# Kernel tuning notes

Measured on AMD Instinct MI355X. Metric: run time of the kernel, lower is better.

The kernel has to match this reference:

```python
import jax, jax.numpy as jnp
import numpy as np

D = 2048
H = 16
DH = D // H  # 128
B = 512
EPS = 1e-5


def _layernorm(x, g, b):
    m = jnp.mean(x, axis=-1, keepdims=True)
    v = jnp.mean((x - m) ** 2, axis=-1, keepdims=True)
    return (x - m) * jax.lax.rsqrt(v + EPS) * g + b


def setup_inputs() -> dict:
    key = jax.random.key(0)
    ks = jax.random.split(key, 16)
    s_in = 1.0 / np.sqrt(D)
    s_ff = 1.0 / np.sqrt(4 * D)
    return {
        "x": jax.random.normal(ks[0], (B, D), jnp.float32),
        # per-head q/k/v projections, stacked over heads: [H, D, DH]
        "Wq": jax.random.uniform(ks[1], (H, D, DH), jnp.float32, -s_in, s_in),
        "bq": jax.random.uniform(ks[2], (H, DH), jnp.float32, -s_in, s_in),
        "Wk": jax.random.uniform(ks[3], (H, D, DH), jnp.float32, -s_in, s_in),
        "bk": jax.random.uniform(ks[4], (H, DH), jnp.float32, -s_in, s_in),
        "Wv": jax.random.uniform(ks[5], (H, D, DH), jnp.float32, -s_in, s_in),
        "bv": jax.random.uniform(ks[6], (H, DH), jnp.float32, -s_in, s_in),
        "Wo": jax.random.uniform(ks[7], (D, D), jnp.float32, -s_in, s_in),
        "bo": jax.random.uniform(ks[8], (D,), jnp.float32, -s_in, s_in),
        "W1": jax.random.uniform(ks[9], (D, 4 * D), jnp.float32, -s_in, s_in),
        "b1": jax.random.uniform(ks[10], (4 * D,), jnp.float32, -s_in, s_in),
        "W2": jax.random.uniform(ks[11], (4 * D, D), jnp.float32, -s_ff, s_ff),
        "b2": jax.random.uniform(ks[12], (D,), jnp.float32, -s_ff, s_ff),
        "g1": jnp.ones((D,), jnp.float32),
        "be1": jnp.zeros((D,), jnp.float32),
        "g2": jnp.ones((D,), jnp.float32),
        "be2": jnp.zeros((D,), jnp.float32),
    }


def reference(x, Wq, bq, Wk, bk, Wv, bv, Wo, bo, W1, b1, W2, b2, g1, be1, g2, be2):
    # --- pre-norm attention branch ---
    h = _layernorm(x, g1, be1)                       # [B, D]
    q = jnp.einsum('bd,hde->bhe', h, Wq) + bq        # [B, H, DH]
    k = jnp.einsum('bd,hde->bhe', h, Wk) + bk
    v = jnp.einsum('bd,hde->bhe', h, Wv) + bv
    # outer-product 'attention' per sample: [B, H, DH, DH]
    attn = q[..., :, None] * k[..., None, :] / jnp.sqrt(jnp.float32(DH))
    attn = jax.nn.softmax(attn, axis=-1)
    o = jnp.einsum('bhij,bhj->bhi', attn, v)         # [B, H, DH]
    o = o.reshape(x.shape[0], H * DH)                # concat over heads
    x = x + o @ Wo + bo
    # --- pre-norm FFN branch ---
    h2 = _layernorm(x, g2, be2)
    x = x + jax.nn.relu(h2 @ W1 + b1) @ W2 + b2
    return x
```

## Files before the change

kernel.cpp:

```cpp
#include <hip/hip_runtime.h>
#include <hip/hip_bf16.h>
#include <math.h>


#define DDIM 2048
#define HHEADS 16
#define DHEAD 128
#define BROWS 512
#define LN_EPS 1e-5f

typedef __bf16 bf16x8_t __attribute__((ext_vector_type(8)));
typedef float f32x4_t __attribute__((ext_vector_type(4)));

#define GLD16(gptr, lptr)                                                     \
    __builtin_amdgcn_global_load_lds(                                         \
        (const __attribute__((address_space(1))) void*)(gptr),                \
        (__attribute__((address_space(3))) void*)(lptr), 16, 0, 0)

__global__ __launch_bounds__(256) void ln_kernel(const float* __restrict__ x,
                                                 const float* __restrict__ g,
                                                 const float* __restrict__ b,
                                                 __bf16* __restrict__ out) {
    const int row = blockIdx.x;
    const int tid = threadIdx.x;
    const float4* x4 = (const float4*)(x + (size_t)row * DDIM);
    float4 a = x4[2 * tid];
    float4 c = x4[2 * tid + 1];
    float s  = a.x + a.y + a.z + a.w + c.x + c.y + c.z + c.w;
    float s2 = a.x*a.x + a.y*a.y + a.z*a.z + a.w*a.w
             + c.x*c.x + c.y*c.y + c.z*c.z + c.w*c.w;
    #pragma unroll
    for (int off = 32; off > 0; off >>= 1) {
        s  += __shfl_down(s, off);
        s2 += __shfl_down(s2, off);
    }
    __shared__ float ps[4], ps2[4];
    __shared__ float mean_s, rstd_s;
    const int lane = tid & 63, w = tid >> 6;
    if (lane == 0) { ps[w] = s; ps2[w] = s2; }
    __syncthreads();
    if (tid == 0) {
        float S  = ps[0] + ps[1] + ps[2] + ps[3];
        float S2 = ps2[0] + ps2[1] + ps2[2] + ps2[3];
        float m  = S * (1.0f / DDIM);
        float var = S2 * (1.0f / DDIM) - m * m;
        mean_s = m;
        rstd_s = rsqrtf(var + LN_EPS);
    }
    __syncthreads();
    const float m = mean_s, r = rstd_s;
    const float4* g4 = (const float4*)g;
    const float4* b4 = (const float4*)b;
    float4 ga = g4[2 * tid], gb = g4[2 * tid + 1];
    float4 ba = b4[2 * tid], bb = b4[2 * tid + 1];
    bf16x8_t o;
    o[0] = (__bf16)((a.x - m) * r * ga.x + ba.x);
    o[1] = (__bf16)((a.y - m) * r * ga.y + ba.y);
    o[2] = (__bf16)((a.z - m) * r * ga.z + ba.z);
    o[3] = (__bf16)((a.w - m) * r * ga.w + ba.w);
    o[4] = (__bf16)((c.x - m) * r * gb.x + bb.x);
    o[5] = (__bf16)((c.y - m) * r * gb.y + bb.y);
    o[6] = (__bf16)((c.z - m) * r * gb.z + bb.z);
    o[7] = (__bf16)((c.w - m) * r * gb.w + bb.w);
    *(bf16x8_t*)(out + (size_t)row * DDIM + tid * 8) = o;
}

__global__ __launch_bounds__(256) void transpose_kernel(
    const float* __restrict__ src, __bf16* __restrict__ dst, int R, int C) {
    __shared__ float tile[64][65];
    const size_t bofs = (size_t)blockIdx.z * R * C;
    src += bofs;
    dst += bofs;
    const int c0 = blockIdx.x * 64, r0 = blockIdx.y * 64;
    const int t = threadIdx.x;
    const int rr = t >> 4, cc = (t & 15) * 4;
    #pragma unroll
    for (int p = 0; p < 4; p++) {
        const float4 v =
            *(const float4*)(src + (size_t)(r0 + rr + 16 * p) * C + c0 + cc);
        tile[rr + 16 * p][cc]     = v.x;
        tile[rr + 16 * p][cc + 1] = v.y;
        tile[rr + 16 * p][cc + 2] = v.z;
        tile[rr + 16 * p][cc + 3] = v.w;
    }
    __syncthreads();
    const int slot = t & 7;
    #pragma unroll
    for (int p = 0; p < 2; p++) {
        const int c = (t >> 3) + 32 * p;
        bf16x8_t o;
        #pragma unroll
        for (int j = 0; j < 8; j++)
            o[j] = (__bf16)tile[slot * 8 + j][c];
        *(bf16x8_t*)(dst + (size_t)(c0 + c) * R + r0 + slot * 8) = o;
    }
}

__global__ __launch_bounds__(256) void fuse_bias_kernel(
    const float* __restrict__ bq, const float* __restrict__ bk,
    const float* __restrict__ bv, float* __restrict__ fb) {
    const int i = blockIdx.x * 256 + threadIdx.x;
    float v;
    if (i < 2048) v = bq[i];
    else if (i < 4096) v = bk[i - 2048];
    else v = bv[i - 4096];
    fb[i] = v;
}

template <int TM, int TN, int DEPTH, int SPLITZ, int OUT_BF16, int RELU, int RES>
__global__ __launch_bounds__(256) void gemm_bt(
    const __bf16* __restrict__ A, int K,
    const __bf16* __restrict__ Bt,
    const float* __restrict__ bias,
    const float* __restrict__ Res,
    void* __restrict__ Cout, int N) {
    constexpr int STG = (TM + TN) * 64;
    __shared__ __align__(16) __bf16 smem[DEPTH * STG];

    const int tid = threadIdx.x;
    const int w = tid >> 6, lane = tid & 63;
    const int m0 = blockIdx.y * TM, n0 = blockIdx.x * TN;

    const int Kloc = K / SPLITZ;
    const int kb = blockIdx.z * Kloc;
    const int NK = Kloc / 64;

    constexpr int NT = (TM + TN) / 8;
    constexpr int NI = NT / 4;

    const int srow = lane >> 3;
    const int sslot = (lane & 7) ^ srow;

    const __bf16* srcs[NI];
    int toff[NI];
    #pragma unroll
    for (int i = 0; i < NI; i++) {
        const int t = w + 4 * i;
        toff[i] = t * 512;
        const int r = t * 8 + srow;
        srcs[i] = (r < TM)
                      ? A + (size_t)(m0 + r) * K + kb + sslot * 8
                      : Bt + (size_t)(n0 + r - TM) * K + kb + sslot * 8;
    }

    constexpr int MI = TM / 32;
    constexpr int NJ = TN / 32;
    const int wm = (w >> 1) * (TM / 2), wn = (w & 1) * (TN / 2);
    const int fm = lane & 15, quad = lane >> 4;
    const int f7 = fm & 7;

    int aoff[2][MI], boff[2][NJ];
    #pragma unroll
    for (int h = 0; h < 2; h++) {
        const int sl = ((h * 4 + quad) ^ f7) * 16;
        #pragma unroll
        for (int i = 0; i < MI; i++)
            aoff[h][i] = (wm + 16 * i + fm) * 128 + sl;
        #pragma unroll
        for (int j = 0; j < NJ; j++)
            boff[h][j] = (TM + wn + 16 * j + fm) * 128 + sl;
    }

    f32x4_t acc[MI][NJ] = {};

    #pragma unroll
    for (int d = 0; d < DEPTH; d++)
        #pragma unroll
        for (int i = 0; i < NI; i++)
            GLD16(srcs[i] + d * 64, smem + d * STG + toff[i]);

    for (int ks = 0; ks < NK; ks++) {
        const char* st = (const char*)smem + (ks % DEPTH) * (STG * 2);
        asm volatile("s_waitcnt vmcnt(%0)\n\ts_barrier"
                     :: "i"((DEPTH - 1) * NI) : "memory");

        bf16x8_t a[2][MI], b[2][NJ];
        #pragma unroll
        for (int h = 0; h < 2; h++) {
            #pragma unroll
            for (int i = 0; i < MI; i++)
                a[h][i] = *(const bf16x8_t*)(st + aoff[h][i]);
            #pragma unroll
            for (int j = 0; j < NJ; j++)
                b[h][j] = *(const bf16x8_t*)(st + boff[h][j]);
        }
        #pragma unroll
        for (int i = 0; i < MI; i++)
            #pragma unroll
            for (int j = 0; j < NJ; j++) {
                acc[i][j] = __builtin_amdgcn_mfma_f32_16x16x32_bf16(
                    a[0][i], b[0][j], acc[i][j], 0, 0, 0);
                acc[i][j] = __builtin_amdgcn_mfma_f32_16x16x32_bf16(
                    a[1][i], b[1][j], acc[i][j], 0, 0, 0);
            }

        asm volatile("s_waitcnt lgkmcnt(0)\n\ts_barrier" ::: "memory");
        if (ks + DEPTH < NK) {
            __bf16* dst = smem + (ks % DEPTH) * STG;
            #pragma unroll
            for (int i = 0; i < NI; i++)
                GLD16(srcs[i] + (size_t)(ks + DEPTH) * 64, dst + toff[i]);
        }
    }

    if (SPLITZ > 1) {
        float* P = (float*)Cout + (size_t)blockIdx.z * (gridDim.y * TM) * N;
        #pragma unroll
        for (int i = 0; i < MI; i++)
            #pragma unroll
            for (int j = 0; j < NJ; j++) {
                const int col = n0 + wn + 16 * j + fm;
                #pragma unroll
                for (int r = 0; r < 4; r++) {
                    const int row = m0 + wm + 16 * i + quad * 4 + r;
                    P[(size_t)row * N + col] = acc[i][j][r];
                }
            }
    } else {
        #pragma unroll
        for (int i = 0; i < MI; i++)
            #pragma unroll
            for (int j = 0; j < NJ; j++) {
                const int col = n0 + wn + 16 * j + fm;
                const float bcol = bias[col];
                #pragma unroll
                for (int r = 0; r < 4; r++) {
                    const int row = m0 + wm + 16 * i + quad * 4 + r;
                    float val = acc[i][j][r] + bcol;
                    if (RES) val += Res[(size_t)row * N + col];
                    if (RELU) val = fmaxf(val, 0.0f);
                    if (OUT_BF16)
                        ((__bf16*)Cout)[(size_t)row * N + col] = (__bf16)val;
                    else
                        ((float*)Cout)[(size_t)row * N + col] = val;
                }
            }
    }
}

template <int NS>
__global__ __launch_bounds__(256) void reduce_splitk(
    const float* __restrict__ part, const float* __restrict__ Res,
    const float* __restrict__ bias, float* __restrict__ out) {
    const int idx = blockIdx.x * 256 + threadIdx.x;
    const float4 b4 = ((const float4*)bias)[idx & 511];
    float4 r = ((const float4*)Res)[idx];
    #pragma unroll
    for (int s = 0; s < NS; s++) {
        const float4 p = ((const float4*)part)[(size_t)s * 262144 + idx];
        r.x += p.x; r.y += p.y; r.z += p.z; r.w += p.w;
    }
    r.x += b4.x; r.y += b4.y; r.z += b4.z; r.w += b4.w;
    ((float4*)out)[idx] = r;
}

__global__ __launch_bounds__(128) void attn_kernel(
    const __bf16* __restrict__ qkv, __bf16* __restrict__ o) {
    const int bh = blockIdx.x;
    const int b = bh >> 4, h = bh & 15;
    const size_t base = (size_t)b * (3 * DDIM) + h * DHEAD;
    const int tid = threadIdx.x;
    __shared__ float ks[DHEAD], vs[DHEAD];
    ks[tid] = (float)qkv[base + DDIM + tid];
    vs[tid] = (float)qkv[base + 2 * DDIM + tid];
    __syncthreads();
    const float a = (float)qkv[base + tid] * 0.08838834764831845f;
    float den = 0.0f, num = 0.0f;
    #pragma unroll 8
    for (int j = 0; j < DHEAD; j++) {
        float e = __expf(a * ks[j]);
        den += e;
        num += e * vs[j];
    }
    o[(size_t)b * DDIM + h * DHEAD + tid] = (__bf16)(num / den);
}

extern "C" void kernel_launch(void* const* d_in, const int* in_sizes, int n_in,
                              void* d_out, int out_size, void* d_ws, size_t ws_size,
                              hipStream_t stream) {
    const float* x   = (const float*)d_in[0];
    const float* Wq  = (const float*)d_in[1];
    const float* bq  = (const float*)d_in[2];
    const float* Wk  = (const float*)d_in[3];
    const float* bk  = (const float*)d_in[4];
    const float* Wv  = (const float*)d_in[5];
    const float* bv  = (const float*)d_in[6];
    const float* Wo  = (const float*)d_in[7];
    const float* bo  = (const float*)d_in[8];
    const float* W1  = (const float*)d_in[9];
    const float* b1  = (const float*)d_in[10];
    const float* W2  = (const float*)d_in[11];
    const float* b2  = (const float*)d_in[12];
    const float* g1  = (const float*)d_in[13];
    const float* be1 = (const float*)d_in[14];
    const float* g2  = (const float*)d_in[15];
    const float* be2 = (const float*)d_in[16];
    float* out = (float*)d_out;

    char* base = (char*)d_ws;
    float*  fb     = (float*)(base + 0);
    __bf16* bt_qkv = (__bf16*)(base + 32768);
    char*   slotA  = base + 32768 + 25165824;
    char*   slotB  = slotA + 33554432;
    __bf16* h   = (__bf16*)(slotB + 0);
    __bf16* qkv = (__bf16*)(slotB + 2097152);
    __bf16* ob  = (__bf16*)(slotB + 8388608);
    float*  woP = (float*)(slotB + 10485760);
    float*  w2P = (float*)(slotB + 0);
    float*  x1  = (float*)((char*)bt_qkv + 0);
    __bf16* h2  = (__bf16*)((char*)bt_qkv + 4194304);
    __bf16* t   = (__bf16*)((char*)bt_qkv + 6291456);
    __bf16* Wot = (__bf16*)slotA;
    __bf16* W1t = (__bf16*)slotB;
    __bf16* W2t = (__bf16*)slotA;

    fuse_bias_kernel<<<24, 256, 0, stream>>>(bq, bk, bv, fb);

    transpose_kernel<<<dim3(2, 32, 16), 256, 0, stream>>>(Wq, bt_qkv, DDIM, DHEAD);
    transpose_kernel<<<dim3(2, 32, 16), 256, 0, stream>>>(Wk, bt_qkv + 2048 * 2048, DDIM, DHEAD);
    transpose_kernel<<<dim3(2, 32, 16), 256, 0, stream>>>(Wv, bt_qkv + 2 * 2048 * 2048, DDIM, DHEAD);
    transpose_kernel<<<dim3(32, 32, 1), 256, 0, stream>>>(Wo, Wot, DDIM, DDIM);

    ln_kernel<<<BROWS, 256, 0, stream>>>(x, g1, be1, h);

    gemm_bt<128, 128, 3, 1, 1, 0, 0><<<dim3(48, 4), 256, 0, stream>>>(
        h, DDIM, bt_qkv, fb, nullptr, qkv, 3 * DDIM);

    attn_kernel<<<BROWS * HHEADS, 128, 0, stream>>>(qkv, ob);

    gemm_bt<64, 128, 4, 2, 0, 0, 0><<<dim3(16, 8, 2), 256, 0, stream>>>(
        ob, DDIM, Wot, nullptr, nullptr, woP, DDIM);
    reduce_splitk<2><<<1024, 256, 0, stream>>>(woP, x, bo, x1);

    transpose_kernel<<<dim3(128, 32, 1), 256, 0, stream>>>(W1, W1t, DDIM, 4 * DDIM);
    transpose_kernel<<<dim3(32, 128, 1), 256, 0, stream>>>(W2, W2t, 4 * DDIM, DDIM);

    ln_kernel<<<BROWS, 256, 0, stream>>>(x1, g2, be2, h2);

    gemm_bt<128, 128, 3, 1, 1, 1, 0><<<dim3(64, 4), 256, 0, stream>>>(
        h2, DDIM, W1t, b1, nullptr, t, 4 * DDIM);

    gemm_bt<128, 128, 3, 4, 0, 0, 0><<<dim3(16, 4, 4), 256, 0, stream>>>(
        t, 4 * DDIM, W2t, nullptr, nullptr, w2P, DDIM);
    reduce_splitk<4><<<1024, 256, 0, stream>>>(w2P, x1, b2, out);
}
```

Before: 367.4 us.

## Use 512-thread GEMM with intra-block K split and fuse reduce with LayerNorm

The GEMM goes to 512 threads, with two groups of four waves each taking one half of every 64-wide K step. The two partial accumulators are merged through LDS before the epilogue. The Wo GEMM becomes 128x128 split-K 4, and its reduction is fused with the second LayerNorm so x1 is not reread. The three QKV weight transposes merge into one launch, and the bias-fusion kernel is replaced by per-segment bias selection in the epilogue. Risks are extra register and LDS pressure, lower occupancy, the added merge cost, and more partial-sum traffic for the Wo GEMM.

```diff
diff --git a/kernel.cpp b/kernel.cpp
--- a/kernel.cpp
+++ b/kernel.cpp
@@ -96,24 +96,49 @@
     }
 }
 
-__global__ __launch_bounds__(256) void fuse_bias_kernel(
-    const float* __restrict__ bq, const float* __restrict__ bk,
-    const float* __restrict__ bv, float* __restrict__ fb) {
-    const int i = blockIdx.x * 256 + threadIdx.x;
-    float v;
-    if (i < 2048) v = bq[i];
-    else if (i < 4096) v = bk[i - 2048];
-    else v = bv[i - 4096];
-    fb[i] = v;
-}
-
-template <int TM, int TN, int DEPTH, int SPLITZ, int OUT_BF16, int RELU, int RES>
-__global__ __launch_bounds__(256) void gemm_bt(
+__global__ __launch_bounds__(256) void transpose_qkv_kernel(
+    const float* __restrict__ Wq, const float* __restrict__ Wk,
+    const float* __restrict__ Wv, __bf16* __restrict__ dstall) {
+    __shared__ float tile[64][65];
+    const int z = blockIdx.z, which = z >> 4, hd = z & 15;
+    const float* src = (which == 0) ? Wq : (which == 1) ? Wk : Wv;
+    src += (size_t)hd * DDIM * DHEAD;
+    __bf16* dst = dstall + (size_t)which * DDIM * DDIM + (size_t)hd * DDIM * DHEAD;
+    const int R = DDIM, C = DHEAD;
+    const int c0 = blockIdx.x * 64, r0 = blockIdx.y * 64;
+    const int t = threadIdx.x;
+    const int rr = t >> 4, cc = (t & 15) * 4;
+    #pragma unroll
+    for (int p = 0; p < 4; p++) {
+        const float4 v =
+            *(const float4*)(src + (size_t)(r0 + rr + 16 * p) * C + c0 + cc);
+        tile[rr + 16 * p][cc]     = v.x;
+        tile[rr + 16 * p][cc + 1] = v.y;
+        tile[rr + 16 * p][cc + 2] = v.z;
+        tile[rr + 16 * p][cc + 3] = v.w;
+    }
+    __syncthreads();
+    const int slot = t & 7;
+    #pragma unroll
+    for (int p = 0; p < 2; p++) {
+        const int c = (t >> 3) + 32 * p;
+        bf16x8_t o;
+        #pragma unroll
+        for (int j = 0; j < 8; j++)
+            o[j] = (__bf16)tile[slot * 8 + j][c];
+        *(bf16x8_t*)(dst + (size_t)(c0 + c) * R + r0 + slot * 8) = o;
+    }
+}
+
+template <int DEPTH, int SPLITZ, int OUT_BF16, int RELU, int RES, int BIAS3>
+__global__ __launch_bounds__(512) void gemm_bt(
     const __bf16* __restrict__ A, int K,
     const __bf16* __restrict__ Bt,
-    const float* __restrict__ bias,
+    const float* __restrict__ bias, const float* __restrict__ biasB,
+    const float* __restrict__ biasC,
     const float* __restrict__ Res,
     void* __restrict__ Cout, int N) {
+    constexpr int TM = 128, TN = 128;
     constexpr int STG = (TM + TN) * 64;
     __shared__ __align__(16) __bf16 smem[DEPTH * STG];
 
@@ -126,7 +151,7 @@
     const int NK = Kloc / 64;
 
     constexpr int NT = (TM + TN) / 8;
-    constexpr int NI = NT / 4;
+    constexpr int NI = NT / 8;
 
     const int srow = lane >> 3;
     const int sslot = (lane & 7) ^ srow;
@@ -135,7 +160,7 @@
     int toff[NI];
     #pragma unroll
     for (int i = 0; i < NI; i++) {
-        const int t = w + 4 * i;
+        const int t = w + 8 * i;
         toff[i] = t * 512;
         const int r = t * 8 + srow;
         srcs[i] = (r < TM)
@@ -143,23 +168,20 @@
                       : Bt + (size_t)(n0 + r - TM) * K + kb + sslot * 8;
     }
 
-    constexpr int MI = TM / 32;
-    constexpr int NJ = TN / 32;
-    const int wm = (w >> 1) * (TM / 2), wn = (w & 1) * (TN / 2);
+    constexpr int MI = 4, NJ = 4;
+    const int wg = w & 3, kh = w >> 2;
+    const int wm = (wg >> 1) * 64, wn = (wg & 1) * 64;
     const int fm = lane & 15, quad = lane >> 4;
     const int f7 = fm & 7;
 
-    int aoff[2][MI], boff[2][NJ];
-    #pragma unroll
-    for (int h = 0; h < 2; h++) {
-        const int sl = ((h * 4 + quad) ^ f7) * 16;
-        #pragma unroll
-        for (int i = 0; i < MI; i++)
-            aoff[h][i] = (wm + 16 * i + fm) * 128 + sl;
-        #pragma unroll
-        for (int j = 0; j < NJ; j++)
-            boff[h][j] = (TM + wn + 16 * j + fm) * 128 + sl;
-    }
+    const int sl = ((kh * 4 + quad) ^ f7) * 16;
+    int aoff[MI], boff[NJ];
+    #pragma unroll
+    for (int i = 0; i < MI; i++)
+        aoff[i] = (wm + 16 * i + fm) * 128 + sl;
+    #pragma unroll
+    for (int j = 0; j < NJ; j++)
+        boff[j] = (TM + wn + 16 * j + fm) * 128 + sl;
 
     f32x4_t acc[MI][NJ] = {};
 
@@ -174,25 +196,19 @@
         asm volatile("s_waitcnt vmcnt(%0)\n\ts_barrier"
                      :: "i"((DEPTH - 1) * NI) : "memory");
 
-        bf16x8_t a[2][MI], b[2][NJ];
-        #pragma unroll
-        for (int h = 0; h < 2; h++) {
-            #pragma unroll
-            for (int i = 0; i < MI; i++)
-                a[h][i] = *(const bf16x8_t*)(st + aoff[h][i]);
+        bf16x8_t a[MI], b[NJ];
+        #pragma unroll
+        for (int i = 0; i < MI; i++)
+            a[i] = *(const bf16x8_t*)(st + aoff[i]);
+        #pragma unroll
+        for (int j = 0; j < NJ; j++)
+            b[j] = *(const bf16x8_t*)(st + boff[j]);
+        #pragma unroll
+        for (int i = 0; i < MI; i++)
             #pragma unroll
             for (int j = 0; j < NJ; j++)
-                b[h][j] = *(const bf16x8_t*)(st + boff[h][j]);
-        }
-        #pragma unroll
-        for (int i = 0; i < MI; i++)
-            #pragma unroll
-            for (int j = 0; j < NJ; j++) {
                 acc[i][j] = __builtin_amdgcn_mfma_f32_16x16x32_bf16(
-                    a[0][i], b[0][j], acc[i][j], 0, 0, 0);
-                acc[i][j] = __builtin_amdgcn_mfma_f32_16x16x32_bf16(
-                    a[1][i], b[1][j], acc[i][j], 0, 0, 0);
-            }
+                    a[i], b[j], acc[i][j], 0, 0, 0);
 
         asm volatile("s_waitcnt lgkmcnt(0)\n\ts_barrier" ::: "memory");
         if (ks + DEPTH < NK) {
@@ -202,6 +218,25 @@
                 GLD16(srcs[i] + (size_t)(ks + DEPTH) * 64, dst + toff[i]);
         }
     }
+
+    char* mrg = (char*)smem + wg * 16384;
+    if (kh == 1) {
+        #pragma unroll
+        for (int i = 0; i < MI; i++)
+            #pragma unroll
+            for (int j = 0; j < NJ; j++)
+                *(f32x4_t*)(mrg + (((i * NJ + j) * 64) + lane) * 16) = acc[i][j];
+    }
+    __syncthreads();
+    if (kh == 1) return;
+    #pragma unroll
+    for (int i = 0; i < MI; i++)
+        #pragma unroll
+        for (int j = 0; j < NJ; j++) {
+            const f32x4_t p = *(const f32x4_t*)(mrg + (((i * NJ + j) * 64) + lane) * 16);
+            acc[i][j][0] += p[0]; acc[i][j][1] += p[1];
+            acc[i][j][2] += p[2]; acc[i][j][3] += p[3];
+        }
 
     if (SPLITZ > 1) {
         float* P = (float*)Cout + (size_t)blockIdx.z * (gridDim.y * TM) * N;
@@ -217,12 +252,17 @@
                 }
             }
     } else {
+        const float* bp = bias;
+        if (BIAS3) {
+            const int seg = n0 >> 11;
+            bp = (seg == 0) ? bias : (seg == 1) ? biasB : biasC;
+        }
         #pragma unroll
         for (int i = 0; i < MI; i++)
             #pragma unroll
             for (int j = 0; j < NJ; j++) {
                 const int col = n0 + wn + 16 * j + fm;
-                const float bcol = bias[col];
+                const float bcol = BIAS3 ? bp[col & 2047] : bp[col];
                 #pragma unroll
                 for (int r = 0; r < 4; r++) {
                     const int row = m0 + wm + 16 * i + quad * 4 + r;
@@ -252,6 +292,69 @@
     }
     r.x += b4.x; r.y += b4.y; r.z += b4.z; r.w += b4.w;
     ((float4*)out)[idx] = r;
+}
+
+template <int NS>
+__global__ __launch_bounds__(256) void reduce_ln_kernel(
+    const float* __restrict__ part, const float* __restrict__ x,
+    const float* __restrict__ bo, const float* __restrict__ g,
+    const float* __restrict__ be, float* __restrict__ x1,
+    __bf16* __restrict__ h2) {
+    const int row = blockIdx.x;
+    const int tid = threadIdx.x;
+    const size_t rbase = (size_t)row * DDIM;
+    float v[8];
+    #pragma unroll
+    for (int p = 0; p < 2; p++) {
+        const int c = tid * 8 + p * 4;
+        float4 r = *(const float4*)(x + rbase + c);
+        const float4 b4 = *(const float4*)(bo + c);
+        r.x += b4.x; r.y += b4.y; r.z += b4.z; r.w += b4.w;
+        #pragma unroll
+        for (int s = 0; s < NS; s++) {
+            const float4 q = *(const float4*)(part + (size_t)s * BROWS * DDIM + rbase + c);
+            r.x += q.x; r.y += q.y; r.z += q.z; r.w += q.w;
+        }
+        *(float4*)(x1 + rbase + c) = r;
+        v[p * 4 + 0] = r.x; v[p * 4 + 1] = r.y; v[p * 4 + 2] = r.z; v[p * 4 + 3] = r.w;
+    }
+    float s = 0.f, s2 = 0.f;
+    #pragma unroll
+    for (int i = 0; i < 8; i++) { s += v[i]; s2 += v[i] * v[i]; }
+    #pragma unroll
+    for (int off = 32; off > 0; off >>= 1) {
+        s  += __shfl_down(s, off);
+        s2 += __shfl_down(s2, off);
+    }
+    __shared__ float ps[4], ps2[4];
+    __shared__ float mean_s, rstd_s;
+    const int lane = tid & 63, wv = tid >> 6;
+    if (lane == 0) { ps[wv] = s; ps2[wv] = s2; }
+    __syncthreads();
+    if (tid == 0) {
+        float S  = ps[0] + ps[1] + ps[2] + ps[3];
+        float S2 = ps2[0] + ps2[1] + ps2[2] + ps2[3];
+        float m  = S * (1.0f / DDIM);
+        float var = S2 * (1.0f / DDIM) - m * m;
+        mean_s = m;
+        rstd_s = rsqrtf(var + LN_EPS);
+    }
+    __syncthreads();
+    const float m = mean_s, r = rstd_s;
+    const float4* g4 = (const float4*)g;
+    const float4* b4 = (const float4*)be;
+    float4 ga = g4[2 * tid], gb = g4[2 * tid + 1];
+    float4 ba = b4[2 * tid], bb = b4[2 * tid + 1];
+    bf16x8_t o;
+    o[0] = (__bf16)((v[0] - m) * r * ga.x + ba.x);
+    o[1] = (__bf16)((v[1] - m) * r * ga.y + ba.y);
+    o[2] = (__bf16)((v[2] - m) * r * ga.z + ba.z);
+    o[3] = (__bf16)((v[3] - m) * r * ga.w + ba.w);
+    o[4] = (__bf16)((v[4] - m) * r * gb.x + bb.x);
+    o[5] = (__bf16)((v[5] - m) * r * gb.y + bb.y);
+    o[6] = (__bf16)((v[6] - m) * r * gb.z + bb.z);
+    o[7] = (__bf16)((v[7] - m) * r * gb.w + bb.w);
+    *(bf16x8_t*)(h2 + rbase + tid * 8) = o;
 }
 
 __global__ __launch_bounds__(128) void attn_kernel(
@@ -298,7 +401,6 @@
     float* out = (float*)d_out;
 
     char* base = (char*)d_ws;
-    float*  fb     = (float*)(base + 0);
     __bf16* bt_qkv = (__bf16*)(base + 32768);
     char*   slotA  = base + 32768 + 25165824;
     char*   slotB  = slotA + 33554432;
@@ -314,33 +416,27 @@
     __bf16* W1t = (__bf16*)slotB;
     __bf16* W2t = (__bf16*)slotA;
 
-    fuse_bias_kernel<<<24, 256, 0, stream>>>(bq, bk, bv, fb);
-
-    transpose_kernel<<<dim3(2, 32, 16), 256, 0, stream>>>(Wq, bt_qkv, DDIM, DHEAD);
-    transpose_kernel<<<dim3(2, 32, 16), 256, 0, stream>>>(Wk, bt_qkv + 2048 * 2048, DDIM, DHEAD);
-    transpose_kernel<<<dim3(2, 32, 16), 256, 0, stream>>>(Wv, bt_qkv + 2 * 2048 * 2048, DDIM, DHEAD);
+    transpose_qkv_kernel<<<dim3(2, 32, 48), 256, 0, stream>>>(Wq, Wk, Wv, bt_qkv);
     transpose_kernel<<<dim3(32, 32, 1), 256, 0, stream>>>(Wo, Wot, DDIM, DDIM);
 
     ln_kernel<<<BROWS, 256, 0, stream>>>(x, g1, be1, h);
 
-    gemm_bt<128, 128, 3, 1, 1, 0, 0><<<dim3(48, 4), 256, 0, stream>>>(
-        h, DDIM, bt_qkv, fb, nullptr, qkv, 3 * DDIM);
+    gemm_bt<3, 1, 1, 0, 0, 1><<<dim3(48, 4), 512, 0, stream>>>(
+        h, DDIM, bt_qkv, bq, bk, bv, nullptr, qkv, 3 * DDIM);
 
     attn_kernel<<<BROWS * HHEADS, 128, 0, stream>>>(qkv, ob);
 
-    gemm_bt<64, 128, 4, 2, 0, 0, 0><<<dim3(16, 8, 2), 256, 0, stream>>>(
-        ob, DDIM, Wot, nullptr, nullptr, woP, DDIM);
-    reduce_splitk<2><<<1024, 256, 0, stream>>>(woP, x, bo, x1);
+    gemm_bt<3, 4, 0, 0, 0, 0><<<dim3(16, 4, 4), 512, 0, stream>>>(
+        ob, DDIM, Wot, nullptr, nullptr, nullptr, nullptr, woP, DDIM);
+    reduce_ln_kernel<4><<<BROWS, 256, 0, stream>>>(woP, x, bo, g2, be2, x1, h2);
 
     transpose_kernel<<<dim3(128, 32, 1), 256, 0, stream>>>(W1, W1t, DDIM, 4 * DDIM);
     transpose_kernel<<<dim3(32, 128, 1), 256, 0, stream>>>(W2, W2t, 4 * DDIM, DDIM);
 
-    ln_kernel<<<BROWS, 256, 0, stream>>>(x1, g2, be2, h2);
-
-    gemm_bt<128, 128, 3, 1, 1, 1, 0><<<dim3(64, 4), 256, 0, stream>>>(
-        h2, DDIM, W1t, b1, nullptr, t, 4 * DDIM);
-
-    gemm_bt<128, 128, 3, 4, 0, 0, 0><<<dim3(16, 4, 4), 256, 0, stream>>>(
-        t, 4 * DDIM, W2t, nullptr, nullptr, w2P, DDIM);
+    gemm_bt<3, 1, 1, 1, 0, 0><<<dim3(64, 4), 512, 0, stream>>>(
+        h2, DDIM, W1t, b1, nullptr, nullptr, nullptr, t, 4 * DDIM);
+
+    gemm_bt<3, 4, 0, 0, 0, 0><<<dim3(16, 4, 4), 512, 0, stream>>>(
+        t, 4 * DDIM, W2t, nullptr, nullptr, nullptr, nullptr, w2P, DDIM);
     reduce_splitk<4><<<1024, 256, 0, stream>>>(w2P, x1, b2, out);
 }
```

New measurement: 351.8 us. -4.2%, faster.

## Fuse fp32 weight load and bf16 convert into GEMMs, drop transpose kernels

Applied to the files above, without the earlier changes.

Removes the separate transpose/convert kernels for all weight matrices. The GEMM now reads fp32 weights directly in their original layout, converts them to bf16 in registers and writes them swizzled into LDS. It also uses 512-thread blocks split into two K-halves whose partial sums are merged through LDS, plus XCD-aware block remapping. The attention output projection now applies bias and residual in its epilogue without split-K. This avoids the full weight read/write round trip but reads fp32 weights (twice the bytes of bf16) inside the GEMM and adds convert and LDS-store work to the main loop.

```diff
diff --git a/kernel.cpp b/kernel.cpp
--- a/kernel.cpp
+++ b/kernel.cpp
@@ -10,6 +10,8 @@
 #define LN_EPS 1e-5f
 
 typedef __bf16 bf16x8_t __attribute__((ext_vector_type(8)));
+typedef __bf16 bf16x4_t __attribute__((ext_vector_type(4)));
+typedef __bf16 bf16x2_t __attribute__((ext_vector_type(2)));
 typedef float f32x4_t __attribute__((ext_vector_type(4)));
 
 #define GLD16(gptr, lptr)                                                     \
@@ -65,146 +67,186 @@
     *(bf16x8_t*)(out + (size_t)row * DDIM + tid * 8) = o;
 }
 
-__global__ __launch_bounds__(256) void transpose_kernel(
-    const float* __restrict__ src, __bf16* __restrict__ dst, int R, int C) {
-    __shared__ float tile[64][65];
-    const size_t bofs = (size_t)blockIdx.z * R * C;
-    src += bofs;
-    dst += bofs;
-    const int c0 = blockIdx.x * 64, r0 = blockIdx.y * 64;
-    const int t = threadIdx.x;
-    const int rr = t >> 4, cc = (t & 15) * 4;
-    #pragma unroll
-    for (int p = 0; p < 4; p++) {
-        const float4 v =
-            *(const float4*)(src + (size_t)(r0 + rr + 16 * p) * C + c0 + cc);
-        tile[rr + 16 * p][cc]     = v.x;
-        tile[rr + 16 * p][cc + 1] = v.y;
-        tile[rr + 16 * p][cc + 2] = v.z;
-        tile[rr + 16 * p][cc + 3] = v.w;
-    }
-    __syncthreads();
-    const int slot = t & 7;
-    #pragma unroll
-    for (int p = 0; p < 2; p++) {
-        const int c = (t >> 3) + 32 * p;
-        bf16x8_t o;
-        #pragma unroll
-        for (int j = 0; j < 8; j++)
-            o[j] = (__bf16)tile[slot * 8 + j][c];
-        *(bf16x8_t*)(dst + (size_t)(c0 + c) * R + r0 + slot * 8) = o;
-    }
-}
-
-__global__ __launch_bounds__(256) void fuse_bias_kernel(
-    const float* __restrict__ bq, const float* __restrict__ bk,
-    const float* __restrict__ bv, float* __restrict__ fb) {
-    const int i = blockIdx.x * 256 + threadIdx.x;
-    float v;
-    if (i < 2048) v = bq[i];
-    else if (i < 4096) v = bk[i - 2048];
-    else v = bv[i - 4096];
-    fb[i] = v;
-}
-
-template <int TM, int TN, int DEPTH, int SPLITZ, int OUT_BF16, int RELU, int RES>
-__global__ __launch_bounds__(256) void gemm_bt(
+template <int TM, int TN, int SPLITZ, int OUT_BF16, int RELU, int RES, int QKV>
+__global__ __launch_bounds__(512, 4) void gemm_af(
     const __bf16* __restrict__ A, int K,
-    const __bf16* __restrict__ Bt,
-    const float* __restrict__ bias,
-    const float* __restrict__ Res,
+    const float* __restrict__ Bq, const float* __restrict__ Bk,
+    const float* __restrict__ Bv, int ldb,
+    const float* __restrict__ bias, const float* __restrict__ biasB,
+    const float* __restrict__ biasC, const float* __restrict__ Res,
     void* __restrict__ Cout, int N) {
+    constexpr int DEPTH = 3;
     constexpr int STG = (TM + TN) * 64;
     __shared__ __align__(16) __bf16 smem[DEPTH * STG];
 
     const int tid = threadIdx.x;
     const int w = tid >> 6, lane = tid & 63;
-    const int m0 = blockIdx.y * TM, n0 = blockIdx.x * TN;
-
+
+    const int gx = gridDim.x, gy = gridDim.y, gz = gridDim.z;
+    int l = blockIdx.x + gx * (blockIdx.y + gy * blockIdx.z);
+    const int xcd = l & 7;
+    int i0 = l >> 3;
+    const int by = i0 % gy; i0 /= gy;
+    const int bz = i0 % gz; i0 /= gz;
+    const int bx = xcd * (gx >> 3) + i0;
+
+    const int m0 = by * TM, n0 = bx * TN;
     const int Kloc = K / SPLITZ;
-    const int kb = blockIdx.z * Kloc;
+    const int kb = bz * Kloc;
     const int NK = Kloc / 64;
 
-    constexpr int NT = (TM + TN) / 8;
-    constexpr int NI = NT / 4;
-
+    constexpr int LA = TM / 64;
     const int srow = lane >> 3;
     const int sslot = (lane & 7) ^ srow;
-
-    const __bf16* srcs[NI];
-    int toff[NI];
-    #pragma unroll
-    for (int i = 0; i < NI; i++) {
-        const int t = w + 4 * i;
+    const __bf16* srcs[LA];
+    int toff[LA];
+    #pragma unroll
+    for (int i = 0; i < LA; i++) {
+        const int t = w + 8 * i;
         toff[i] = t * 512;
-        const int r = t * 8 + srow;
-        srcs[i] = (r < TM)
-                      ? A + (size_t)(m0 + r) * K + kb + sslot * 8
-                      : Bt + (size_t)(n0 + r - TM) * K + kb + sslot * 8;
-    }
-
-    constexpr int MI = TM / 32;
-    constexpr int NJ = TN / 32;
-    const int wm = (w >> 1) * (TM / 2), wn = (w & 1) * (TN / 2);
+        srcs[i] = A + (size_t)(m0 + t * 8 + srow) * K + kb + sslot * 8;
+    }
+
+    constexpr int KPER = TN / 32;
+    constexpr int LB = KPER;
+    constexpr int NPR = TN / 4;
+    const int np = tid & (NPR - 1);
+    const int kp = tid / NPR;
+    const int k0 = kp * KPER, n0t = np * 4;
+
+    const float* bbase;
+    if (QKV) {
+        const int seg = n0 >> 11;
+        const float* sel = (seg == 0) ? Bq : (seg == 1) ? Bk : Bv;
+        bbase = sel + (size_t)((n0 & 2047) >> 7) * (DDIM * DHEAD);
+    } else {
+        bbase = Bq + n0;
+    }
+    const float* bthr = bbase + (size_t)(kb + k0) * ldb + n0t;
+    const size_t bstep = (size_t)64 * ldb;
+
+    int bwoff[4];
+    {
+        const int bslot = k0 >> 3, bhalf = (k0 & 7) * 2;
+        #pragma unroll
+        for (int j = 0; j < 4; j++) {
+            const int n = n0t + j;
+            const int fb = (n ^ (n >> 2)) & 7;
+            bwoff[j] = (TM + n) * 128 + ((bslot ^ fb) * 16) + bhalf;
+        }
+    }
+
+    constexpr int MI = TM / 32, NJ = TN / 32;
+    const int wg = w & 3, kh = w >> 2;
+    const int wm = (wg >> 1) * (TM / 2), wn = (wg & 1) * (TN / 2);
     const int fm = lane & 15, quad = lane >> 4;
-    const int f7 = fm & 7;
-
-    int aoff[2][MI], boff[2][NJ];
-    #pragma unroll
-    for (int h = 0; h < 2; h++) {
-        const int sl = ((h * 4 + quad) ^ f7) * 16;
+    const int slq = kh * 4 + quad;
+    int aoff[MI], boff[NJ];
+    #pragma unroll
+    for (int i = 0; i < MI; i++)
+        aoff[i] = (wm + 16 * i + fm) * 128 + ((slq ^ (fm & 7)) * 16);
+    #pragma unroll
+    for (int j = 0; j < NJ; j++) {
+        const int n = wn + 16 * j + fm;
+        const int fb = (n ^ (n >> 2)) & 7;
+        boff[j] = (TM + n) * 128 + ((slq ^ fb) * 16);
+    }
+
+    f32x4_t acc[MI][NJ] = {};
+    f32x4_t bufA[KPER], bufB[KPER];
+
+    auto loadB = [&](int ks2, f32x4_t (&dst)[KPER]) {
+        const float* q = bthr + (size_t)ks2 * bstep;
+        #pragma unroll
+        for (int j = 0; j < KPER; j++)
+            dst[j] = *(const f32x4_t*)(q + (size_t)j * ldb);
+    };
+    auto writeB = [&](int slot, const f32x4_t (&src)[KPER]) {
+        char* stg = (char*)smem + slot * (STG * 2);
+        #pragma unroll
+        for (int j = 0; j < 4; j++) {
+            if constexpr (KPER == 4) {
+                bf16x4_t u;
+                u[0] = (__bf16)src[0][j]; u[1] = (__bf16)src[1][j];
+                u[2] = (__bf16)src[2][j]; u[3] = (__bf16)src[3][j];
+                *(bf16x4_t*)(stg + bwoff[j]) = u;
+            } else {
+                bf16x2_t u;
+                u[0] = (__bf16)src[0][j]; u[1] = (__bf16)src[1][j];
+                *(bf16x2_t*)(stg + bwoff[j]) = u;
+            }
+        }
+    };
+
+    loadB(0, bufB);
+    #pragma unroll
+    for (int i = 0; i < LA; i++) GLD16(srcs[i], smem + toff[i]);
+    loadB(1, bufA);
+    #pragma unroll
+    for (int i = 0; i < LA; i++) GLD16(srcs[i] + 64, smem + STG + toff[i]);
+    writeB(0, bufB);
+
+    auto body = [&](int ks, f32x4_t (&wr)[KPER], f32x4_t (&ld)[KPER]) {
+        const int sc = ks % DEPTH;
+        if (ks == 0 || ks == NK - 1)
+            asm volatile("s_waitcnt vmcnt(0) lgkmcnt(0)\n\ts_barrier"
+                         ::: "memory");
+        else
+            asm volatile("s_waitcnt vmcnt(%0) lgkmcnt(0)\n\ts_barrier"
+                         :: "i"(LB + LA) : "memory");
+        if (ks + 2 < NK) {
+            const int s2 = (ks + 2) % DEPTH;
+            loadB(ks + 2, ld);
+            #pragma unroll
+            for (int i = 0; i < LA; i++)
+                GLD16(srcs[i] + (size_t)(ks + 2) * 64,
+                      smem + s2 * STG + toff[i]);
+        }
+        const char* st = (const char*)smem + sc * (STG * 2);
+        bf16x8_t a[MI], b[NJ];
+        #pragma unroll
+        for (int i = 0; i < MI; i++) a[i] = *(const bf16x8_t*)(st + aoff[i]);
+        #pragma unroll
+        for (int j = 0; j < NJ; j++) b[j] = *(const bf16x8_t*)(st + boff[j]);
+        if (ks + 1 < NK) writeB((ks + 1) % DEPTH, wr);
+        __builtin_amdgcn_s_setprio(1);
         #pragma unroll
         for (int i = 0; i < MI; i++)
-            aoff[h][i] = (wm + 16 * i + fm) * 128 + sl;
-        #pragma unroll
-        for (int j = 0; j < NJ; j++)
-            boff[h][j] = (TM + wn + 16 * j + fm) * 128 + sl;
-    }
-
-    f32x4_t acc[MI][NJ] = {};
-
-    #pragma unroll
-    for (int d = 0; d < DEPTH; d++)
-        #pragma unroll
-        for (int i = 0; i < NI; i++)
-            GLD16(srcs[i] + d * 64, smem + d * STG + toff[i]);
-
-    for (int ks = 0; ks < NK; ks++) {
-        const char* st = (const char*)smem + (ks % DEPTH) * (STG * 2);
-        asm volatile("s_waitcnt vmcnt(%0)\n\ts_barrier"
-                     :: "i"((DEPTH - 1) * NI) : "memory");
-
-        bf16x8_t a[2][MI], b[2][NJ];
-        #pragma unroll
-        for (int h = 0; h < 2; h++) {
-            #pragma unroll
-            for (int i = 0; i < MI; i++)
-                a[h][i] = *(const bf16x8_t*)(st + aoff[h][i]);
             #pragma unroll
             for (int j = 0; j < NJ; j++)
-                b[h][j] = *(const bf16x8_t*)(st + boff[h][j]);
-        }
+                acc[i][j] = __builtin_amdgcn_mfma_f32_16x16x32_bf16(
+                    a[i], b[j], acc[i][j], 0, 0, 0);
+        __builtin_amdgcn_s_setprio(0);
+    };
+
+    for (int ks = 0; ks < NK; ks += 2) {
+        body(ks, bufA, bufB);
+        body(ks + 1, bufB, bufA);
+    }
+
+    char* mrg = (char*)smem + wg * (MI * NJ * 64 * 16);
+    __syncthreads();
+    if (kh == 1) {
         #pragma unroll
         for (int i = 0; i < MI; i++)
             #pragma unroll
-            for (int j = 0; j < NJ; j++) {
-                acc[i][j] = __builtin_amdgcn_mfma_f32_16x16x32_bf16(
-                    a[0][i], b[0][j], acc[i][j], 0, 0, 0);
-                acc[i][j] = __builtin_amdgcn_mfma_f32_16x16x32_bf16(
-                    a[1][i], b[1][j], acc[i][j], 0, 0, 0);
-            }
-
-        asm volatile("s_waitcnt lgkmcnt(0)\n\ts_barrier" ::: "memory");
-        if (ks + DEPTH < NK) {
-            __bf16* dst = smem + (ks % DEPTH) * STG;
-            #pragma unroll
-            for (int i = 0; i < NI; i++)
-                GLD16(srcs[i] + (size_t)(ks + DEPTH) * 64, dst + toff[i]);
-        }
-    }
+            for (int j = 0; j < NJ; j++)
+                *(f32x4_t*)(mrg + (((i * NJ + j) * 64) + lane) * 16) = acc[i][j];
+    }
+    __syncthreads();
+    if (kh == 1) return;
+    #pragma unroll
+    for (int i = 0; i < MI; i++)
+        #pragma unroll
+        for (int j = 0; j < NJ; j++) {
+            const f32x4_t p =
+                *(const f32x4_t*)(mrg + (((i * NJ + j) * 64) + lane) * 16);
+            acc[i][j][0] += p[0]; acc[i][j][1] += p[1];
+            acc[i][j][2] += p[2]; acc[i][j][3] += p[3];
+        }
 
     if (SPLITZ > 1) {
-        float* P = (float*)Cout + (size_t)blockIdx.z * (gridDim.y * TM) * N;
+        float* P = (float*)Cout + (size_t)bz * (gy * TM) * N;
         #pragma unroll
         for (int i = 0; i < MI; i++)
             #pragma unroll
@@ -217,12 +259,17 @@
                 }
             }
     } else {
+        const float* bp = bias;
+        if (QKV) {
+            const int seg = n0 >> 11;
+            bp = (seg == 0) ? bias : (seg == 1) ? biasB : biasC;
+        }
         #pragma unroll
         for (int i = 0; i < MI; i++)
             #pragma unroll
             for (int j = 0; j < NJ; j++) {
                 const int col = n0 + wn + 16 * j + fm;
-                const float bcol = bias[col];
+                const float bcol = QKV ? bp[col & 2047] : bp[col];
                 #pragma unroll
                 for (int r = 0; r < 4; r++) {
                     const int row = m0 + wm + 16 * i + quad * 4 + r;
@@ -298,49 +345,34 @@
     float* out = (float*)d_out;
 
     char* base = (char*)d_ws;
-    float*  fb     = (float*)(base + 0);
-    __bf16* bt_qkv = (__bf16*)(base + 32768);
-    char*   slotA  = base + 32768 + 25165824;
-    char*   slotB  = slotA + 33554432;
-    __bf16* h   = (__bf16*)(slotB + 0);
-    __bf16* qkv = (__bf16*)(slotB + 2097152);
-    __bf16* ob  = (__bf16*)(slotB + 8388608);
-    float*  woP = (float*)(slotB + 10485760);
-    float*  w2P = (float*)(slotB + 0);
-    float*  x1  = (float*)((char*)bt_qkv + 0);
-    __bf16* h2  = (__bf16*)((char*)bt_qkv + 4194304);
-    __bf16* t   = (__bf16*)((char*)bt_qkv + 6291456);
-    __bf16* Wot = (__bf16*)slotA;
-    __bf16* W1t = (__bf16*)slotB;
-    __bf16* W2t = (__bf16*)slotA;
-
-    fuse_bias_kernel<<<24, 256, 0, stream>>>(bq, bk, bv, fb);
-
-    transpose_kernel<<<dim3(2, 32, 16), 256, 0, stream>>>(Wq, bt_qkv, DDIM, DHEAD);
-    transpose_kernel<<<dim3(2, 32, 16), 256, 0, stream>>>(Wk, bt_qkv + 2048 * 2048, DDIM, DHEAD);
-    transpose_kernel<<<dim3(2, 32, 16), 256, 0, stream>>>(Wv, bt_qkv + 2 * 2048 * 2048, DDIM, DHEAD);
-    transpose_kernel<<<dim3(32, 32, 1), 256, 0, stream>>>(Wo, Wot, DDIM, DDIM);
+    __bf16* h   = (__bf16*)(base + 0);
+    __bf16* qkv = (__bf16*)(base + 2097152);
+    __bf16* ob  = (__bf16*)(base + 8388608);
+    float*  x1  = (float*)(base + 10485760);
+    __bf16* h2  = (__bf16*)(base + 14680064);
+    __bf16* t   = (__bf16*)(base + 16777216);
+    float*  w2P = (float*)(base + 25165824);
 
     ln_kernel<<<BROWS, 256, 0, stream>>>(x, g1, be1, h);
 
-    gemm_bt<128, 128, 3, 1, 1, 0, 0><<<dim3(48, 4), 256, 0, stream>>>(
-        h, DDIM, bt_qkv, fb, nullptr, qkv, 3 * DDIM);
+    gemm_af<64, 128, 1, 1, 0, 0, 1><<<dim3(48, 8), 512, 0, stream>>>(
+        h, DDIM, Wq, Wk, Wv, DHEAD, bq, bk, bv, nullptr, qkv, 3 * DDIM);
 
     attn_kernel<<<BROWS * HHEADS, 128, 0, stream>>>(qkv, ob);
 
-    gemm_bt<64, 128, 4, 2, 0, 0, 0><<<dim3(16, 8, 2), 256, 0, stream>>>(
-        ob, DDIM, Wot, nullptr, nullptr, woP, DDIM);
-    reduce_splitk<2><<<1024, 256, 0, stream>>>(woP, x, bo, x1);
-
-    transpose_kernel<<<dim3(128, 32, 1), 256, 0, stream>>>(W1, W1t, DDIM, 4 * DDIM);
-    transpose_kernel<<<dim3(32, 128, 1), 256, 0, stream>>>(W2, W2t, 4 * DDIM, DDIM);
+    gemm_af<64, 64, 1, 0, 0, 1, 0><<<dim3(32, 8), 512, 0, stream>>>(
+        ob, DDIM, Wo, nullptr, nullptr, DDIM, bo, nullptr, nullptr, x,
+        x1, DDIM);
 
     ln_kernel<<<BROWS, 256, 0, stream>>>(x1, g2, be2, h2);
 
-    gemm_bt<128, 128, 3, 1, 1, 1, 0><<<dim3(64, 4), 256, 0, stream>>>(
-        h2, DDIM, W1t, b1, nullptr, t, 4 * DDIM);
-
-    gemm_bt<128, 128, 3, 4, 0, 0, 0><<<dim3(16, 4, 4), 256, 0, stream>>>(
-        t, 4 * DDIM, W2t, nullptr, nullptr, w2P, DDIM);
+    gemm_af<64, 128, 1, 1, 1, 0, 0><<<dim3(64, 8), 512, 0, stream>>>(
+        h2, DDIM, W1, nullptr, nullptr, 4 * DDIM, b1, nullptr, nullptr,
+        nullptr, t, 4 * DDIM);
+
+    gemm_af<64, 128, 4, 0, 0, 0, 0><<<dim3(16, 8, 4), 512, 0, stream>>>(
+        t, 4 * DDIM, W2, nullptr, nullptr, DDIM, nullptr, nullptr, nullptr,
+        nullptr, w2P, DDIM);
+
     reduce_splitk<4><<<1024, 256, 0, stream>>>(w2P, x1, b2, out);
 }
```

Result: slower. 459.6 us (+25.1%).
